# Kernel optimization log

Measured on AMD Instinct MI355X. Metric: run time of the kernel, lower is better.

## Reference

```python
import jax, jax.numpy as jnp
import numpy as np

B, S, IN, H, OUT, L = 32, 512, 300, 180, 60, 4
NBLOCK, NF = 3, 3  # mel_smooth_layers, mel_smooth_filter_size
GRP = OUT // NF    # 20 groups per mel conv


def setup_inputs() -> dict:
    key = jax.random.key(0)
    ks = jax.random.split(key, 12)
    def u(k, shape, scale):
        return jax.random.uniform(k, shape, jnp.float32, -scale, scale)
    s = float(1.0 / np.sqrt(H))
    return {
        "x": jax.random.normal(ks[0], (B, S, IN), jnp.float32),
        "Wih0": u(ks[1], (4 * H, IN), s),
        "Wih_rest": u(ks[2], (L - 1, 4 * H, H), s),
        "Whh": u(ks[3], (L, 4 * H, H), s),
        "bih": u(ks[4], (L, 4 * H), s),
        "bhh": u(ks[5], (L, 4 * H), s),
        "linW": u(ks[6], (OUT, H), s),
        "linb": u(ks[7], (OUT,), s),
        "mel_w": u(ks[8], (NBLOCK, NF, GRP, NF, 5), 0.2),  # per block, per filter: Conv1d(60,20,5,groups=20)
        "mel_b": u(ks[9], (NBLOCK, NF, GRP), 0.2),
        "resW": u(ks[10], (OUT, 2, 5), 0.2),               # Conv1d(120,60,5,groups=60)
        "resb": u(ks[11], (OUT,), 0.2),
    }


def _lstm(x, Wih0, Wih_rest, Whh, bih, bhh):
    # torch nn.LSTM, batch_first, gate order (i, f, g, o)
    h_in = x  # [B, S, D]
    for l in range(L):
        Wih = Wih0 if l == 0 else Wih_rest[l - 1]
        Whh_l = Whh[l]
        b = bih[l] + bhh[l]
        xt = h_in.transpose(1, 0, 2) @ Wih.T + b  # [S, B, 4H], input projection hoisted out of scan
        def step(carry, xg):
            h, c = carry
            g = xg + h @ Whh_l.T
            i, f, gg, o = jnp.split(g, 4, axis=-1)
            c = jax.nn.sigmoid(f) * c + jax.nn.sigmoid(i) * jnp.tanh(gg)
            h = jax.nn.sigmoid(o) * jnp.tanh(c)
            return (h, c), h
        init = (jnp.zeros((x.shape[0], H), x.dtype), jnp.zeros((x.shape[0], H), x.dtype))
        _, hs = jax.lax.scan(step, init, xt)  # [S, B, H]
        h_in = hs.transpose(1, 0, 2)
    return h_in  # [B, S, H]


def _conv1d_grouped(x, w, b, groups):
    # x: [B, C, S], w: [O, C//groups, K]
    y = jax.lax.conv_general_dilated(
        x, w, window_strides=(1,), padding=[(2, 2)],
        dimension_numbers=("NCH", "OIH", "NCH"), feature_group_count=groups)
    return y + b[None, :, None]


def _mel_block(x, w, b):
    # x: [B, 60, S]; w: [NF, 20, NF, 5]; b: [NF, 20]
    Bb, C, Ss = x.shape
    z = jnp.zeros((Bb, 1, Ss), x.dtype)
    # shifted channel stacks: [down-shift-1, identity, up-shift-1] (filter_size_channel == 3)
    xs = [jnp.concatenate([z, x[:, :-1]], axis=1), x, jnp.concatenate([x[:, 1:], z], axis=1)]
    outs = [_conv1d_grouped(xs[j], w[j], b[j], GRP) for j in range(NF)]  # each [B, 20, S]
    # interleave: output channel 3*i + j = outs[j][:, i, :]
    return jnp.stack(outs, axis=2).reshape(Bb, C, Ss)


def _forward(x, Wih0, Wih_rest, Whh, bih, bhh, linW, linb, mel_w, mel_b, resW, resb):
    h = _lstm(x, Wih0, Wih_rest, Whh, bih, bhh)      # [B, S, H]
    out = h @ linW.T + linb                          # [B, S, 60]
    out = out.transpose(0, 2, 1)                     # [B, 60, S]
    lstm_out = out
    for l in range(NBLOCK):
        out = _mel_block(out, mel_w[l], mel_b[l]) + out  # block + shortcut (Identity activation)
    # interleave (lstm, smoothed) per mel channel -> [B, 120, S]
    pair = jnp.stack([lstm_out, out], axis=2).reshape(out.shape[0], 2 * OUT, out.shape[2])
    out = _conv1d_grouped(pair, resW, resb, OUT)     # [B, 60, S]
    return out.transpose(0, 2, 1)                    # [B, S, 60] (Identity output activation)


def reference(x, Wih0, Wih_rest, Whh, bih, bhh, linW, linb, mel_w, mel_b, resW, resb):
    return _forward(x, Wih0, Wih_rest, Whh, bih, bhh, linW, linb, mel_w, mel_b, resW, resb)
```

## Files before the change

### kernel.cpp

```cpp
#include <hip/hip_runtime.h>
#include <hip/hip_bf16.h>

#define B_ 32
#define S_ 512
#define IN_ 300
#define H_ 180
#define G4_ 720
#define OUT_ 60
#define R_ 16384
#define TC_ 32
#define NC_ 16
#define NPK_ 92

#define PWHH_O  0u
#define PW0_O   264960u
#define PWR_O   372960u
#define BIASF_O 567360u
#define LINWF_O 570240u
#define LINBF_O 581040u
#define WFT_    581100u

#define XG_O   0u
#define HR_O   5898240u
#define H3_O   7004160u
#define WFU_O  8478720u
#define STH_O  9059820u
#define STC_O  9082860u
#define FLAG_O 9105900u
#define XGSLOT 737280
#define HRSLOT 184320

#if defined(__has_builtin)
#if __has_builtin(__builtin_amdgcn_fdot2)
#define HAVE_FDOT2 1
#endif
#endif

typedef _Float16 f16x2 __attribute__((ext_vector_type(2)));

struct Plan {
  int nl; int ll[4]; int lc[4];
  int ng; int gl[4]; int gc[4];
};

__device__ __forceinline__ float sigf(float x)   { return 1.f / (1.f + __expf(-x)); }
__device__ __forceinline__ float tanhf2(float x) { return 2.f / (1.f + __expf(-2.f * x)) - 1.f; }
__device__ __forceinline__ float toF(__hip_bfloat16 x) { return __bfloat162float(x); }
__device__ __forceinline__ float ldr(const void* p, long i, int fl) {
  return fl ? ((const float*)p)[i] : toF(((const __hip_bfloat16*)p)[i]);
}
__device__ __forceinline__ unsigned f16b(_Float16 h) {
  union { _Float16 f; unsigned short s; } x; x.f = h; return x.s;
}
__device__ __forceinline__ float h2f(unsigned s) {
  union { unsigned short s; _Float16 f; } x; x.s = (unsigned short)(s & 0xFFFFu);
  return (float)x.f;
}
__device__ __forceinline__ f16x2 u2h(unsigned u) {
  union { unsigned u; f16x2 v; } x; x.u = u; return x.v;
}
__device__ __forceinline__ float fd2(unsigned hu, unsigned wu, float acc) {
#ifdef HAVE_FDOT2
  return __builtin_amdgcn_fdot2(u2h(hu), u2h(wu), acc, false);
#else
  return acc + h2f(hu) * h2f(wu) + h2f(hu >> 16) * h2f(wu >> 16);
#endif
}
__device__ __forceinline__ unsigned packpair_f32(float lo, float hi) {
  return f16b((_Float16)lo) | (f16b((_Float16)hi) << 16);
}
__device__ __forceinline__ unsigned packpair_bf16(unsigned u) {
  union { unsigned v; float f; } a, b;
  a.v = u << 16; b.v = u & 0xFFFF0000u;
  return packpair_f32(a.f, b.f);
}

#define REP23(M) M(0) M(1) M(2) M(3) M(4) M(5) M(6) M(7) M(8) M(9) M(10) \
  M(11) M(12) M(13) M(14) M(15) M(16) M(17) M(18) M(19) M(20) M(21) M(22)
#define LW(n) \
  unsigned w##n##a = wp0[(4*n+0)*G4_], w##n##b = wp0[(4*n+1)*G4_], \
           w##n##c = wp0[(4*n+2)*G4_], w##n##d = wp0[(4*n+3)*G4_];
#define PW(n) \
  asm volatile("" : "+v"(w##n##a), "+v"(w##n##b), "+v"(w##n##c), "+v"(w##n##d));
#define ST(n) { \
  const uint4 hh = *(const uint4*)&hpk[4*n]; \
  a0 = fd2(hh.x, w##n##a, a0); a1 = fd2(hh.y, w##n##b, a1); \
  a2 = fd2(hh.z, w##n##c, a2); a3 = fd2(hh.w, w##n##d, a3); }

__global__ __launch_bounds__(256) void detect_kernel(
    const unsigned short* __restrict__ xw, int* __restrict__ flag) {
  __shared__ int cnt;
  if (threadIdx.x == 0) cnt = 0;
  __syncthreads();
  int lc = 0;
  for (int i = threadIdx.x; i < 2048; i += 256) {
    const int e = (xw[i] >> 7) & 0xFF;
    if (e >= 0xC0 || (e > 0 && e < 0x40)) lc++;
  }
  atomicAdd(&cnt, lc);
  __syncthreads();
  if (threadIdx.x == 0) *flag = (cnt > 100) ? 1 : 0;
}

__global__ __launch_bounds__(256) void prep_kernel(
    const void* __restrict__ wih0, const void* __restrict__ wihr,
    const void* __restrict__ whh,  const void* __restrict__ bih,
    const void* __restrict__ bhh,  const void* __restrict__ linw,
    const void* __restrict__ linb, float* __restrict__ wf,
    const int* __restrict__ flag) {
  const unsigned i = blockIdx.x * 256u + threadIdx.x;
  if (i >= WFT_) return;
  const int fl = *flag;
  if (i < PW0_O) {
    const unsigned l = i / 66240u, r = i % 66240u;
    const unsigned jp = r / 720u, o = r % 720u;
    unsigned u = 0u;
    if (jp < 90u) {
      const long b = (long)l * 129600 + (long)o * H_;
      u = packpair_f32(ldr(whh, b + 2 * jp, fl), ldr(whh, b + 2 * jp + 1, fl));
    }
    ((unsigned*)wf)[i] = u;
    return;
  }
  if (i < PWR_O) {
    const unsigned j = i - PW0_O, o = j / 150u, kp = j % 150u;
    const long b = (long)o * IN_;
    ((unsigned*)wf)[i] =
        packpair_f32(ldr(wih0, b + 2 * kp, fl), ldr(wih0, b + 2 * kp + 1, fl));
    return;
  }
  if (i < BIASF_O) {
    const unsigned j = i - PWR_O, l = j / 64800u, r = j % 64800u;
    const unsigned o = r / 90u, kp = r % 90u;
    const long b = (long)l * 129600 + (long)o * H_;
    ((unsigned*)wf)[i] =
        packpair_f32(ldr(wihr, b + 2 * kp, fl), ldr(wihr, b + 2 * kp + 1, fl));
    return;
  }
  float v;
  if (i < LINWF_O)      { const unsigned j = i - BIASF_O; v = ldr(bih, j, fl) + ldr(bhh, j, fl); }
  else if (i < LINBF_O) v = ldr(linw, i - LINWF_O, fl);
  else                  v = ldr(linb, i - LINBF_O, fl);
  wf[i] = v;
}

__global__ __launch_bounds__(768, 3) void fused_kernel(
    const void* __restrict__ x, const int* __restrict__ flag,
    const unsigned* __restrict__ wfu,
    float* __restrict__ xg, float* __restrict__ hr,
    __hip_bfloat16* __restrict__ h3,
    float* __restrict__ sth, float* __restrict__ stc, Plan p) {
  __shared__ __align__(16) unsigned hpk[NPK_];
  __shared__ float gbuf[G4_];
  __shared__ __align__(16) unsigned Asu[3][10][68];
  __shared__ __align__(16) unsigned Bsu[3][10][68];

  const int bid = blockIdx.x;
  if (bid < p.nl * 32) {
    const int j = bid >> 5, b = bid & 31;
    const int l = p.ll[j], c = p.lc[j];
    const int o = threadIdx.x;
    const bool act = o < G4_;
    const int oc = act ? o : 0;
    const unsigned* wp0 = wfu + PWHH_O + (unsigned)l * (NPK_ * G4_) + oc;
    REP23(LW)
    REP23(PW)
    const float* xgs = xg + (long)(l * 2 + (c & 1)) * XGSLOT;
    float* hrs = hr + (long)((l < 3 ? l : 0) * 2 + (c & 1)) * HRSLOT;
    float cst = 0.f;
    if (o == 180 || o == 181) hpk[o - 90] = 0u;
    if (o < H_) {
      float h = 0.f;
      if (c != 0) { h = sth[(l * 32 + b) * H_ + o]; cst = stc[(l * 32 + b) * H_ + o]; }
      const unsigned v = f16b((_Float16)h);
      const unsigned nx = __shfl_down(v, 1);
      if ((o & 1) == 0) hpk[o >> 1] = v | (nx << 16);
    }
    const float* xgp = xgs + (long)b * TC_ * G4_ + oc;
    float xcur = xgp[0];
    __syncthreads();
    for (int tl = 0; tl < TC_; ++tl) {
      {
        float a0 = xcur, a1 = 0.f, a2 = 0.f, a3 = 0.f;
        REP23(ST)
        const float acc = (a0 + a1) + (a2 + a3);
        const bool isg = (o >= 2 * H_) && (o < 3 * H_);
        if (act) gbuf[o] = isg ? tanhf2(acc) : sigf(acc);
        const int tn = (tl + 1 < TC_) ? tl + 1 : tl;
        xcur = xgp[(long)tn * G4_];
      }
      __syncthreads();
      if (o < H_) {
        cst = gbuf[H_ + o] * cst + gbuf[o] * gbuf[2 * H_ + o];
        const float h = gbuf[3 * H_ + o] * tanhf2(cst);
        if (l < 3) hrs[(b * TC_ + tl) * H_ + o] = h;
        else h3[((long)b * S_ + c * TC_ + tl) * H_ + o] = __float2bfloat16(h);
        const unsigned v = f16b((_Float16)h);
        const unsigned nx = __shfl_down(v, 1);
        if ((o & 1) == 0) hpk[o >> 1] = v | (nx << 16);
        if (tl == TC_ - 1) {
          sth[(l * 32 + b) * H_ + o] = h; stc[(l * 32 + b) * H_ + o] = cst;
        }
      }
      __syncthreads();
    }
    return;
  }

  const int gb = bid - p.nl * 32;
  const int g = threadIdx.x >> 8, t = threadIdx.x & 255;
  const int ti = gb * 3 + g;
  const int jj = ti / 192, idx = ti % 192;
  const int rt = idx & 15, ct = idx >> 4;
  const int l = p.gl[jj], c = p.gc[jj];
  const int fl = *flag;
  const int KP = (l == 0) ? 150 : 90;
  const unsigned* Wp = (l == 0) ? (wfu + PW0_O)
                                : (wfu + PWR_O + (unsigned)(l - 1) * 64800u);
  const float* bias = (const float*)wfu + BIASF_O + (unsigned)l * G4_;
  const float* hA = (l == 0) ? nullptr
                  : hr + (long)((l - 1) * 2 + (c & 1)) * HRSLOT;
  float* dst = xg + (long)(l * 2 + (c & 1)) * XGSLOT;
  const int rho0 = rt * 64, o0 = ct * 64;
  const int tx = t & 15, ty = t >> 4;
  float acc[4][4] = {};
  for (int kp0 = 0; kp0 < KP; kp0 += 10) {
    for (int e = t; e < 640; e += 256) {
      const int rl = e / 10, pp = e % 10;
      const int rho = rho0 + rl;
      unsigned av;
      if (l == 0) {
        const int bb = rho >> 5, tl = rho & 31;
        const long gr = (long)bb * S_ + c * TC_ + tl;
        if (fl == 0) av = packpair_bf16(((const unsigned*)x)[gr * 150 + kp0 + pp]);
        else { const float2 f = ((const float2*)x)[gr * 150 + kp0 + pp];
               av = packpair_f32(f.x, f.y); }
      } else {
        const float2 f = ((const float2*)hA)[(long)rho * 90 + kp0 + pp];
        av = packpair_f32(f.x, f.y);
      }
      Asu[g][pp][rl] = av;
      const int o = o0 + rl;
      Bsu[g][pp][rl] = (o < G4_) ? Wp[(long)o * KP + kp0 + pp] : 0u;
    }
    __syncthreads();
#pragma unroll
    for (int pp = 0; pp < 10; ++pp) {
      const uint4 a4 = *(const uint4*)&Asu[g][pp][ty * 4];
      const uint4 b4 = *(const uint4*)&Bsu[g][pp][tx * 4];
      const unsigned av[4] = {a4.x, a4.y, a4.z, a4.w};
      const unsigned bv[4] = {b4.x, b4.y, b4.z, b4.w};
#pragma unroll
      for (int i = 0; i < 4; ++i)
#pragma unroll
        for (int j2 = 0; j2 < 4; ++j2) acc[i][j2] = fd2(av[i], bv[j2], acc[i][j2]);
    }
    __syncthreads();
  }
#pragma unroll
  for (int i = 0; i < 4; ++i) {
    const int rho = rho0 + ty * 4 + i;
#pragma unroll
    for (int j2 = 0; j2 < 4; ++j2) {
      const int o = o0 + tx * 4 + j2;
      if (o < G4_) dst[(long)rho * G4_ + o] = acc[i][j2] + bias[o];
    }
  }
}

__global__ __launch_bounds__(256) void linear_kernel(
    const __hip_bfloat16* __restrict__ h, const float* __restrict__ linw,
    const float* __restrict__ linb, float* __restrict__ out) {
  __shared__ __align__(16) float Ast[20][68];
  __shared__ __align__(16) float Bst[20][68];
  const int bt = blockIdx.x;
  const int b = bt >> 3, st0 = (bt & 7) * 64;
  const int t = threadIdx.x, tx = t & 15, ty = t >> 4;
  float acc[4][4] = {};
  for (int k0 = 0; k0 < H_; k0 += 20) {
    for (int e = t; e < 1280; e += 256) {
      const int rl = e / 20, kk = e % 20;
      Ast[kk][rl] = toF(h[(long)(b * S_ + st0 + rl) * H_ + k0 + kk]);
      Bst[kk][rl] = (rl < OUT_) ? linw[rl * H_ + k0 + kk] : 0.f;
    }
    __syncthreads();
#pragma unroll
    for (int kk = 0; kk < 20; ++kk) {
      const float4 a4 = *(const float4*)&Ast[kk][ty * 4];
      const float4 b4 = *(const float4*)&Bst[kk][tx * 4];
      const float av[4] = {a4.x, a4.y, a4.z, a4.w};
      const float bv[4] = {b4.x, b4.y, b4.z, b4.w};
#pragma unroll
      for (int i = 0; i < 4; ++i)
#pragma unroll
        for (int j2 = 0; j2 < 4; ++j2) acc[i][j2] += av[i] * bv[j2];
    }
    __syncthreads();
  }
#pragma unroll
  for (int i = 0; i < 4; ++i) {
    const int s = st0 + ty * 4 + i;
#pragma unroll
    for (int j2 = 0; j2 < 4; ++j2) {
      const int c = tx * 4 + j2;
      if (c < OUT_) out[((long)b * OUT_ + c) * S_ + s] = acc[i][j2] + linb[c];
    }
  }
}

__global__ __launch_bounds__(256) void mel_kernel(
    const float* __restrict__ in, float* __restrict__ out,
    const void* __restrict__ mw, const void* __restrict__ mb,
    int l, const int* __restrict__ flag) {
  const int fl = *flag;
  const int idx = blockIdx.x;
  const int s = (idx & 1) * 256 + threadIdx.x;
  const int c = (idx >> 1) % OUT_;
  const int b = idx / (2 * OUT_);
  const int j = c % 3, i = c / 3;
  float acc = ldr(mb, (l * 3 + j) * 20 + i, fl);
  const long wbase = (long)((l * 3 + j) * 20 + i) * 15;
#pragma unroll
  for (int q = 0; q < 3; ++q) {
    const int ch = 3 * i + q + j - 1;
    if (ch < 0 || ch >= OUT_) continue;
    const float* xr = in + ((long)b * OUT_ + ch) * S_;
#pragma unroll
    for (int k = 0; k < 5; ++k) {
      const int sp = s + k - 2;
      if (sp < 0 || sp >= S_) continue;
      acc += ldr(mw, wbase + q * 5 + k, fl) * xr[sp];
    }
  }
  out[((long)b * OUT_ + c) * S_ + s] = acc + in[((long)b * OUT_ + c) * S_ + s];
}

__global__ __launch_bounds__(256) void res_kernel(
    const float* __restrict__ lin, const float* __restrict__ mel,
    const void* __restrict__ rw, const void* __restrict__ rb,
    void* __restrict__ outp, const int* __restrict__ flag) {
  const int fl = *flag;
  const int q = threadIdx.x >> 6, lane = threadIdx.x & 63;
  const int bs = blockIdx.x * 4 + q;
  const int b = bs / S_, s = bs % S_;
  if (lane >= OUT_) return;
  const int c = lane;
  float acc = ldr(rb, c, fl);
  const float* x0 = lin + ((long)b * OUT_ + c) * S_;
  const float* x1 = mel + ((long)b * OUT_ + c) * S_;
#pragma unroll
  for (int k = 0; k < 5; ++k) {
    const int sp = s + k - 2;
    if (sp < 0 || sp >= S_) continue;
    acc += ldr(rw, c * 10 + k, fl) * x0[sp] + ldr(rw, c * 10 + 5 + k, fl) * x1[sp];
  }
  const long oi = (long)bs * OUT_ + c;
  if (fl == 0) ((__hip_bfloat16*)outp)[oi] = __float2bfloat16(acc);
  else ((float*)outp)[oi] = acc;
}

extern "C" void kernel_launch(void* const* d_in, const int* in_sizes, int n_in,
                              void* d_out, int out_size, void* d_ws, size_t ws_size,
                              hipStream_t stream) {
  const void* x    = d_in[0];
  const void* wih0 = d_in[1];
  const void* wihr = d_in[2];
  const void* whh  = d_in[3];
  const void* bih  = d_in[4];
  const void* bhh  = d_in[5];
  const void* linw = d_in[6];
  const void* linb = d_in[7];
  const void* melw = d_in[8];
  const void* melb = d_in[9];
  const void* resw = d_in[10];
  const void* resb = d_in[11];

  float* ws = (float*)d_ws;
  float* xg = ws + XG_O;
  float* hrp = ws + HR_O;
  __hip_bfloat16* h3 = (__hip_bfloat16*)(ws + H3_O);
  float* wf = ws + WFU_O;
  const unsigned* wfu = (const unsigned*)wf;
  float* sth = ws + STH_O;
  float* stc = ws + STC_O;
  int* flag = (int*)(ws + FLAG_O);
  float* lin = ws + XG_O;
  float* m1 = lin + 983040;
  float* m2 = m1 + 983040;

  detect_kernel<<<1, 256, 0, stream>>>((const unsigned short*)x, flag);
  prep_kernel<<<(WFT_ + 255) / 256, 256, 0, stream>>>(
      wih0, wihr, whh, bih, bhh, linw, linb, wf, flag);

  {
    Plan p = {};
    p.nl = 0; p.ng = 1; p.gl[0] = 0; p.gc[0] = 0;
    fused_kernel<<<64, 768, 0, stream>>>(x, flag, wfu, xg, hrp, h3, sth, stc, p);
  }
  for (int n = 0; n <= 21; ++n) {
    Plan p = {};
    for (int l = 0; l < 4; ++l) {
      const int c = n - 2 * l;
      if (c >= 0 && c < NC_) { p.ll[p.nl] = l; p.lc[p.nl] = c; p.nl++; }
    }
    for (int l = 0; l < 4; ++l) {
      const int c = n + 1 - 2 * l;
      if (c >= 0 && c < NC_) { p.gl[p.ng] = l; p.gc[p.ng] = c; p.ng++; }
    }
    const int grid = p.nl * 32 + p.ng * 64;
    fused_kernel<<<grid, 768, 0, stream>>>(x, flag, wfu, xg, hrp, h3, sth, stc, p);
  }

  linear_kernel<<<256, 256, 0, stream>>>(h3, wf + LINWF_O, wf + LINBF_O, lin);
  mel_kernel<<<B_ * OUT_ * 2, 256, 0, stream>>>(lin, m1, melw, melb, 0, flag);
  mel_kernel<<<B_ * OUT_ * 2, 256, 0, stream>>>(m1, m2, melw, melb, 1, flag);
  mel_kernel<<<B_ * OUT_ * 2, 256, 0, stream>>>(m2, m1, melw, melb, 2, flag);
  res_kernel<<<R_ / 4, 256, 0, stream>>>(lin, m1, resw, resb, d_out, flag);
}
```

Before: 1.509 ms.

## Batch LSTM recurrence across 16 sequences per block using MFMA f16 matmuls

The recurrent step used to run one block per batch element, doing per-thread fdot2 dot products over the hidden state. It now runs two blocks per layer chunk, each handling 16 batch rows, and computes h@Whh^T with 16x16x32 f16 MFMA instructions. Whh is pre-packed into MFMA B-fragment layout held in registers, and h is double-buffered in swizzled LDS so each step needs only one barrier. The input-projection GEMM now writes xg in a layout matching the MFMA accumulators so gate math stays in registers. The cost is far fewer blocks on the serial critical path and a larger register footprint per thread.

```diff
diff --git a/kernel.cpp b/kernel.cpp
--- a/kernel.cpp
+++ b/kernel.cpp
@@ -10,24 +10,23 @@
 #define R_ 16384
 #define TC_ 32
 #define NC_ 16
-#define NPK_ 92
-
-#define PWHH_O  0u
-#define PW0_O   264960u
-#define PWR_O   372960u
-#define BIASF_O 567360u
-#define LINWF_O 570240u
-#define LINBF_O 581040u
-#define WFT_    581100u
+
+#define BFRAG_O 0u
+#define PW0_O   294912u
+#define PWR_O   402912u
+#define BIASF_O 597312u
+#define LINWF_O 600192u
+#define LINBF_O 610992u
+#define WFT_    611052u
 
 #define XG_O   0u
-#define HR_O   5898240u
-#define H3_O   7004160u
-#define WFU_O  8478720u
-#define STH_O  9059820u
-#define STC_O  9082860u
-#define FLAG_O 9105900u
-#define XGSLOT 737280
+#define HR_O   6291456u
+#define H3_O   7397376u
+#define WFU_O  8871936u
+#define STH_O  9482988u
+#define STC_O  9506028u
+#define FLAG_O 9530604u
+#define XGSLOT 786432
 #define HRSLOT 184320
 
 #if defined(__has_builtin)
@@ -37,6 +36,10 @@
 #endif
 
 typedef _Float16 f16x2 __attribute__((ext_vector_type(2)));
+typedef _Float16 f16x8 __attribute__((ext_vector_type(8)));
+typedef float f32x4 __attribute__((ext_vector_type(4)));
+
+union U16x8 { uint4 u; f16x8 h; };
 
 struct Plan {
   int nl; int ll[4]; int lc[4];
@@ -75,17 +78,23 @@
   return packpair_f32(a.f, b.f);
 }
 
-#define REP23(M) M(0) M(1) M(2) M(3) M(4) M(5) M(6) M(7) M(8) M(9) M(10) \
-  M(11) M(12) M(13) M(14) M(15) M(16) M(17) M(18) M(19) M(20) M(21) M(22)
-#define LW(n) \
-  unsigned w##n##a = wp0[(4*n+0)*G4_], w##n##b = wp0[(4*n+1)*G4_], \
-           w##n##c = wp0[(4*n+2)*G4_], w##n##d = wp0[(4*n+3)*G4_];
-#define PW(n) \
-  asm volatile("" : "+v"(w##n##a), "+v"(w##n##b), "+v"(w##n##c), "+v"(w##n##d));
-#define ST(n) { \
-  const uint4 hh = *(const uint4*)&hpk[4*n]; \
-  a0 = fd2(hh.x, w##n##a, a0); a1 = fd2(hh.y, w##n##b, a1); \
-  a2 = fd2(hh.z, w##n##c, a2); a3 = fd2(hh.w, w##n##d, a3); }
+#define REPGS(M) \
+  M(0,0) M(0,1) M(0,2) M(0,3) M(0,4) M(0,5) \
+  M(1,0) M(1,1) M(1,2) M(1,3) M(1,4) M(1,5) \
+  M(2,0) M(2,1) M(2,2) M(2,3) M(2,4) M(2,5) \
+  M(3,0) M(3,1) M(3,2) M(3,3) M(3,4) M(3,5)
+
+#define LBF(g,s) \
+  U16x8 ub##g##_##s; ub##g##_##s.u = bfp[((g) * 6 + (s)) * 64]; \
+  f16x8 B##g##_##s = ub##g##_##s.h; \
+  asm volatile("" : "+v"(B##g##_##s));
+
+#define MST(s) { \
+  const f16x8 av = *(const f16x8*)(hbc + (li * 384 + (((q * 16) + (s) * 64) ^ ((li & 7) << 4)))); \
+  a0 = __builtin_amdgcn_mfma_f32_16x16x32_f16(av, B0_##s, a0, 0, 0, 0); \
+  a1 = __builtin_amdgcn_mfma_f32_16x16x32_f16(av, B1_##s, a1, 0, 0, 0); \
+  a2 = __builtin_amdgcn_mfma_f32_16x16x32_f16(av, B2_##s, a2, 0, 0, 0); \
+  a3 = __builtin_amdgcn_mfma_f32_16x16x32_f16(av, B3_##s, a3, 0, 0, 0); }
 
 __global__ __launch_bounds__(256) void detect_kernel(
     const unsigned short* __restrict__ xw, int* __restrict__ flag) {
@@ -112,14 +121,20 @@
   if (i >= WFT_) return;
   const int fl = *flag;
   if (i < PW0_O) {
-    const unsigned l = i / 66240u, r = i % 66240u;
-    const unsigned jp = r / 720u, o = r % 720u;
-    unsigned u = 0u;
-    if (jp < 90u) {
-      const long b = (long)l * 129600 + (long)o * H_;
-      u = packpair_f32(ldr(whh, b + 2 * jp, fl), ldr(whh, b + 2 * jp + 1, fl));
-    }
-    ((unsigned*)wf)[i] = u;
+    const unsigned l = i / 73728u, idx = i % 73728u;
+    const unsigned wd = idx & 3u, lane = (idx >> 2) & 63u;
+    const unsigned rest = idx >> 8;
+    const unsigned s = rest % 6u, gq = rest / 6u;
+    const unsigned g = gq & 3u, wv = gq >> 2;
+    const unsigned k0 = s * 32u + ((lane >> 4) << 3) + wd * 2u;
+    const unsigned uu = wv * 16u + (lane & 15u);
+    float v0 = 0.f, v1 = 0.f;
+    if (uu < 180u) {
+      const long b = (long)l * 129600 + (long)(g * 180u + uu) * H_;
+      if (k0 < 180u)      v0 = ldr(whh, b + k0, fl);
+      if (k0 + 1u < 180u) v1 = ldr(whh, b + k0 + 1u, fl);
+    }
+    ((unsigned*)wf)[i] = packpair_f32(v0, v1);
     return;
   }
   if (i < PWR_O) {
@@ -150,64 +165,74 @@
     float* __restrict__ xg, float* __restrict__ hr,
     __hip_bfloat16* __restrict__ h3,
     float* __restrict__ sth, float* __restrict__ stc, Plan p) {
-  __shared__ __align__(16) unsigned hpk[NPK_];
-  __shared__ float gbuf[G4_];
+  __shared__ __align__(16) unsigned short hbf[2 * 16 * 192];
   __shared__ __align__(16) unsigned Asu[3][10][68];
   __shared__ __align__(16) unsigned Bsu[3][10][68];
 
   const int bid = blockIdx.x;
-  if (bid < p.nl * 32) {
-    const int j = bid >> 5, b = bid & 31;
+  if (bid < p.nl * 2) {
+    const int j = bid >> 1, half = bid & 1;
     const int l = p.ll[j], c = p.lc[j];
-    const int o = threadIdx.x;
-    const bool act = o < G4_;
-    const int oc = act ? o : 0;
-    const unsigned* wp0 = wfu + PWHH_O + (unsigned)l * (NPK_ * G4_) + oc;
-    REP23(LW)
-    REP23(PW)
-    const float* xgs = xg + (long)(l * 2 + (c & 1)) * XGSLOT;
-    float* hrs = hr + (long)((l < 3 ? l : 0) * 2 + (c & 1)) * HRSLOT;
-    float cst = 0.f;
-    if (o == 180 || o == 181) hpk[o - 90] = 0u;
-    if (o < H_) {
-      float h = 0.f;
-      if (c != 0) { h = sth[(l * 32 + b) * H_ + o]; cst = stc[(l * 32 + b) * H_ + o]; }
-      const unsigned v = f16b((_Float16)h);
-      const unsigned nx = __shfl_down(v, 1);
-      if ((o & 1) == 0) hpk[o >> 1] = v | (nx << 16);
-    }
-    const float* xgp = xgs + (long)b * TC_ * G4_ + oc;
-    float xcur = xgp[0];
+    const int tid = threadIdx.x;
+    const int w = tid >> 6, lane = tid & 63;
+    const int li = lane & 15, q = lane >> 4;
+    const int u = w * 16 + li;
+    const uint4* bfp = (const uint4*)(wfu + BFRAG_O) +
+                       ((long)l * 18432 + w * 1536 + lane);
+    REPGS(LBF)
+    f32x4* stc4 = (f32x4*)stc;
+    const int sidx = ((l * 2 + half) * 12 + w) * 64 + lane;
+    f32x4 cr = {0.f, 0.f, 0.f, 0.f};
+    if (c != 0) cr = stc4[sidx];
+    float* hrs = (l < 3) ? (hr + (long)(l * 2 + (c & 1)) * HRSLOT) : (float*)0;
+    const f32x4* xgf = (const f32x4*)(xg + (long)(l * 2 + (c & 1)) * XGSLOT);
+    const int xb = (half * 12 + w) * 256 + lane;
+    {
+      char* hbw0 = (char*)hbf;
+      for (int e = tid; e < 16 * 192; e += 768) {
+        const int bb = e / 192, uu = e - bb * 192;
+        float hv = 0.f;
+        if (c != 0 && uu < 180) hv = sth[(l * 32 + half * 16 + bb) * 180 + uu];
+        *(unsigned short*)(hbw0 + bb * 384 + ((uu * 2) ^ ((bb & 7) << 4))) =
+            (unsigned short)f16b((_Float16)hv);
+      }
+    }
+    f32x4 nx0 = xgf[xb], nx1 = xgf[xb + 64], nx2 = xgf[xb + 128], nx3 = xgf[xb + 192];
     __syncthreads();
-    for (int tl = 0; tl < TC_; ++tl) {
-      {
-        float a0 = xcur, a1 = 0.f, a2 = 0.f, a3 = 0.f;
-        REP23(ST)
-        const float acc = (a0 + a1) + (a2 + a3);
-        const bool isg = (o >= 2 * H_) && (o < 3 * H_);
-        if (act) gbuf[o] = isg ? tanhf2(acc) : sigf(acc);
-        const int tn = (tl + 1 < TC_) ? tl + 1 : tl;
-        xcur = xgp[(long)tn * G4_];
+    for (int t = 0; t < TC_; ++t) {
+      const char* hbc = (const char*)hbf + ((t & 1) ? 6144 : 0);
+      char* hbw = (char*)hbf + ((t & 1) ? 0 : 6144);
+      f32x4 a0 = nx0, a1 = nx1, a2 = nx2, a3 = nx3;
+      MST(0) MST(1) MST(2) MST(3) MST(4) MST(5)
+      if (t + 1 < TC_) {
+        const long xi = xb + (long)(t + 1) * 6144;
+        nx0 = xgf[xi]; nx1 = xgf[xi + 64]; nx2 = xgf[xi + 128]; nx3 = xgf[xi + 192];
       }
-      __syncthreads();
-      if (o < H_) {
-        cst = gbuf[H_ + o] * cst + gbuf[o] * gbuf[2 * H_ + o];
-        const float h = gbuf[3 * H_ + o] * tanhf2(cst);
-        if (l < 3) hrs[(b * TC_ + tl) * H_ + o] = h;
-        else h3[((long)b * S_ + c * TC_ + tl) * H_ + o] = __float2bfloat16(h);
-        const unsigned v = f16b((_Float16)h);
-        const unsigned nx = __shfl_down(v, 1);
-        if ((o & 1) == 0) hpk[o >> 1] = v | (nx << 16);
-        if (tl == TC_ - 1) {
-          sth[(l * 32 + b) * H_ + o] = h; stc[(l * 32 + b) * H_ + o] = cst;
+#pragma unroll
+      for (int r = 0; r < 4; ++r) {
+        const float ig = sigf(a0[r]), fg = sigf(a1[r]);
+        const float gg = tanhf2(a2[r]), og = sigf(a3[r]);
+        const float cn = fg * cr[r] + ig * gg;
+        cr[r] = cn;
+        float h = og * tanhf2(cn);
+        if (u >= 180) h = 0.f;
+        const int brow = q * 4 + r;
+        *(unsigned short*)(hbw + brow * 384 + ((u * 2) ^ ((brow & 7) << 4))) =
+            (unsigned short)f16b((_Float16)h);
+        if (u < 180) {
+          const int b = half * 16 + brow;
+          if (l < 3) hrs[(long)(b * TC_ + t) * H_ + u] = h;
+          else       h3[((long)b * S_ + c * TC_ + t) * H_ + u] = __float2bfloat16(h);
+          if (t == TC_ - 1) sth[(l * 32 + b) * H_ + u] = h;
         }
       }
-      __syncthreads();
-    }
+      asm volatile("s_waitcnt lgkmcnt(0)\n\ts_barrier" ::: "memory");
+    }
+    stc4[sidx] = cr;
     return;
   }
 
-  const int gb = bid - p.nl * 32;
+  const int gb = bid - p.nl * 2;
   const int g = threadIdx.x >> 8, t = threadIdx.x & 255;
   const int ti = gb * 3 + g;
   const int jj = ti / 192, idx = ti % 192;
@@ -218,7 +243,7 @@
   const unsigned* Wp = (l == 0) ? (wfu + PW0_O)
                                 : (wfu + PWR_O + (unsigned)(l - 1) * 64800u);
   const float* bias = (const float*)wfu + BIASF_O + (unsigned)l * G4_;
-  const float* hA = (l == 0) ? nullptr
+  const float* hA = (l == 0) ? (const float*)0
                   : hr + (long)((l - 1) * 2 + (c & 1)) * HRSLOT;
   float* dst = xg + (long)(l * 2 + (c & 1)) * XGSLOT;
   const int rho0 = rt * 64, o0 = ct * 64;
@@ -257,14 +282,25 @@
     }
     __syncthreads();
   }
+  int oidx[4], ocol[4];
+#pragma unroll
+  for (int j2 = 0; j2 < 4; ++j2) {
+    const int o = o0 + tx * 4 + j2;
+    ocol[j2] = o;
+    if (o < G4_) {
+      const int gi = o / 180, uu = o - gi * 180;
+      oidx[j2] = (uu >> 4) * 1024 + gi * 256 + (uu & 15) * 4;
+    } else oidx[j2] = -1;
+  }
 #pragma unroll
   for (int i = 0; i < 4; ++i) {
     const int rho = rho0 + ty * 4 + i;
-#pragma unroll
-    for (int j2 = 0; j2 < 4; ++j2) {
-      const int o = o0 + tx * 4 + j2;
-      if (o < G4_) dst[(long)rho * G4_ + o] = acc[i][j2] + bias[o];
-    }
+    const int bb = rho >> 5, tt = rho & 31;
+    const int hf = bb >> 4, bt = bb & 15;
+    const long rowoff = (long)(tt * 2 + hf) * 12288 + (bt >> 2) * 64 + (bt & 3);
+#pragma unroll
+    for (int j2 = 0; j2 < 4; ++j2)
+      if (oidx[j2] >= 0) dst[rowoff + oidx[j2]] = acc[i][j2] + bias[ocol[j2]];
   }
 }
 
@@ -407,7 +443,7 @@
       const int c = n + 1 - 2 * l;
       if (c >= 0 && c < NC_) { p.gl[p.ng] = l; p.gc[p.ng] = c; p.ng++; }
     }
-    const int grid = p.nl * 32 + p.ng * 64;
+    const int grid = p.nl * 2 + p.ng * 64;
     fused_kernel<<<grid, 768, 0, stream>>>(x, flag, wfu, xg, hrp, h3, sth, stc, p);
   }
 
```

Measured after the change: 2.355 ms. +56.0%, slower.
